# Kernel optimization log

Measured on AMD Instinct MI355X. Metric: run time of the kernel, lower is better.

The kernel has to match this reference:

```python
import jax, jax.numpy as jnp
import numpy as np

EPS = 1e-5

def _layernorm(x, gamma, beta):
    # LayerNormalization over last axis (channels), epsilon=1e-5
    mu = jnp.mean(x, axis=-1, keepdims=True)
    var = jnp.var(x, axis=-1, keepdims=True)
    return (x - mu) * jax.lax.rsqrt(var + EPS) * gamma + beta

def setup_inputs() -> dict:
    key = jax.random.key(0)
    ks = jax.random.split(key, 6)
    B, H, W, C = 8, 64, 64, 256
    std = 0.1  # NIN init_scale
    return {
        "x": jax.random.normal(ks[0], (B, H, W, C), dtype=jnp.float32),
        "ln_gamma": jnp.ones((C,), dtype=jnp.float32),
        "ln_beta": jnp.zeros((C,), dtype=jnp.float32),
        "wq": jax.random.normal(ks[1], (C, C), dtype=jnp.float32) * std,
        "bq": jnp.zeros((C,), dtype=jnp.float32),
        "wk": jax.random.normal(ks[2], (C, C), dtype=jnp.float32) * std,
        "bk": jnp.zeros((C,), dtype=jnp.float32),
        "wv": jax.random.normal(ks[3], (C, C), dtype=jnp.float32) * std,
        "bv": jnp.zeros((C,), dtype=jnp.float32),
        "wo": jax.random.normal(ks[4], (C, C), dtype=jnp.float32) * std,
        "bo": jnp.zeros((C,), dtype=jnp.float32),
    }

def reference(x, ln_gamma, ln_beta, wq, bq, wk, bk, wv, bv, wo, bo):
    B, H, W, C = x.shape
    h = _layernorm(x, ln_gamma, ln_beta)
    # 1x1 convs == per-pixel channel matmuls
    q = jnp.einsum('bhwc,cd->bhwd', h, wq) + bq
    k = jnp.einsum('bhwc,cd->bhwd', h, wk) + bk
    v = jnp.einsum('bhwc,cd->bhwd', h, wv) + bv
    scale = jnp.float32(C) ** -0.5
    # dense spatial attention over all H*W tokens
    w = jnp.einsum('bhwc,bijc->bhwij', q, k) * scale  # [B,H,W,H,W]
    w = jax.nn.softmax(w.reshape(B, H, W, H * W), axis=-1).reshape(B, H, W, H, W)
    h = jnp.einsum('bhwij,bijc->bhwc', w, v)
    h = jnp.einsum('bhwc,cd->bhwd', h, wo) + bo
    return x + h
```

## Files before the change

### kernel.cpp

```cpp
#include <hip/hip_runtime.h>
#include <stdint.h>

#define NB    8
#define NTOK  4096
#define TOK   32768
#define CDIM  256
#define BQ    128
#define BK    64
#define NT    (NTOK / BK)

#define KPITCH 264
#define VPITCH 68
#define KTILE_SH (BK * KPITCH)
#define VTILE_SH (CDIM * VPITCH)
#define KCH   33
#define VCH   34
#define TOTCH (KCH + VCH)

typedef __attribute__((ext_vector_type(8))) short bf16x8;
typedef __attribute__((ext_vector_type(4))) float f32x4;

#define SSCALE 0.09016844f

static __device__ __forceinline__ unsigned short f2bf(float f) {
    union { float f; unsigned u; } v; v.f = f;
    unsigned r = v.u + 0x7fffu + ((v.u >> 16) & 1u);
    return (unsigned short)(r >> 16);
}

static __device__ __forceinline__ void dma16(const unsigned short* g, unsigned short* l) {
    __builtin_amdgcn_global_load_lds(
        (const __attribute__((address_space(1))) unsigned int*)g,
        (__attribute__((address_space(3))) unsigned int*)l,
        16, 0, 0);
}

__global__ __launch_bounds__(256) void prep_kernel(
        const float* __restrict__ x,
        const float* __restrict__ gamma,
        const float* __restrict__ beta,
        const float* __restrict__ w0, const float* __restrict__ w1,
        const float* __restrict__ w2, const float* __restrict__ w3,
        unsigned short* __restrict__ h_bf,
        unsigned short* __restrict__ wt) {
    int bx = blockIdx.x;
    if (bx >= TOK / 4) {
        int id = bx - TOK / 4;
        int m = id >> 8, dd = id & 255;
        const float* src = (m == 0) ? w0 : (m == 1) ? w1 : (m == 2) ? w2 : w3;
        wt[m * (CDIM * CDIM) + dd * CDIM + threadIdx.x] = f2bf(src[threadIdx.x * CDIM + dd]);
        return;
    }
    int w = threadIdx.x >> 6;
    int lane = threadIdx.x & 63;
    int token = bx * 4 + w;
    const float4 xv = ((const float4*)(x + (size_t)token * CDIM))[lane];
    float s = xv.x + xv.y + xv.z + xv.w;
    #pragma unroll
    for (int off = 1; off < 64; off <<= 1) s += __shfl_xor(s, off, 64);
    float mean = s * (1.0f / 256.0f);
    float d0 = xv.x - mean, d1 = xv.y - mean, d2 = xv.z - mean, d3 = xv.w - mean;
    float ss = d0 * d0 + d1 * d1 + d2 * d2 + d3 * d3;
    #pragma unroll
    for (int off = 1; off < 64; off <<= 1) ss += __shfl_xor(ss, off, 64);
    float rstd = rsqrtf(ss * (1.0f / 256.0f) + 1e-5f);
    float4 g = ((const float4*)gamma)[lane];
    float4 b = ((const float4*)beta)[lane];
    ushort4 o;
    o.x = f2bf(d0 * rstd * g.x + b.x);
    o.y = f2bf(d1 * rstd * g.y + b.y);
    o.z = f2bf(d2 * rstd * g.z + b.z);
    o.w = f2bf(d3 * rstd * g.w + b.w);
    ((ushort4*)(h_bf + (size_t)token * CDIM))[lane] = o;
}

__global__ __launch_bounds__(128) void qkv_kernel(
        const unsigned short* __restrict__ h_bf,
        const unsigned short* __restrict__ wts,
        const float* __restrict__ bq,
        const float* __restrict__ bk,
        const float* __restrict__ bv,
        unsigned short* __restrict__ q_bf,
        unsigned short* __restrict__ k2,
        unsigned short* __restrict__ vt2) {
    __shared__ unsigned short VT[64][VPITCH];
    int tid = threadIdx.x;
    int w = tid >> 6, lane = tid & 63, quad = lane >> 4, l16 = lane & 15;
    int blk = blockIdx.x;
    int gy = blockIdx.y;
    int nt0 = gy * 4;
    int tok_base = blk * 64 + w * 32;

    bf16x8 afr[2][8];
    #pragma unroll
    for (int s = 0; s < 2; ++s)
        #pragma unroll
        for (int kk = 0; kk < 8; ++kk)
            afr[s][kk] = *(const bf16x8*)(h_bf + (size_t)(tok_base + s * 16 + l16) * CDIM + kk * 32 + quad * 8);

    {
        const unsigned short* wq_t = wts;
        #pragma unroll
        for (int ntl = 0; ntl < 4; ++ntl) {
            int nt = nt0 + ntl;
            f32x4 acc0 = {0.f, 0.f, 0.f, 0.f};
            f32x4 acc1 = {0.f, 0.f, 0.f, 0.f};
            #pragma unroll
            for (int kk = 0; kk < 8; ++kk) {
                bf16x8 bfr = *(const bf16x8*)(wq_t + (size_t)(nt * 16 + l16) * CDIM + kk * 32 + quad * 8);
                acc0 = __builtin_amdgcn_mfma_f32_16x16x32_bf16(afr[0][kk], bfr, acc0, 0, 0, 0);
                acc1 = __builtin_amdgcn_mfma_f32_16x16x32_bf16(afr[1][kk], bfr, acc1, 0, 0, 0);
            }
            int d = nt * 16 + l16;
            float bb = bq[d];
            #pragma unroll
            for (int r = 0; r < 4; ++r) {
                q_bf[(size_t)(tok_base + quad * 4 + r) * CDIM + d]      = f2bf((acc0[r] + bb) * SSCALE);
                q_bf[(size_t)(tok_base + 16 + quad * 4 + r) * CDIM + d] = f2bf((acc1[r] + bb) * SSCALE);
            }
        }
    }
    {
        const unsigned short* wk_t = wts + CDIM * CDIM;
        unsigned short* kdst = k2 + (size_t)blk * KTILE_SH;
        int row0 = w * 32 + quad * 4;
        #pragma unroll
        for (int ntl = 0; ntl < 4; ++ntl) {
            int nt = nt0 + ntl;
            f32x4 acc0 = {0.f, 0.f, 0.f, 0.f};
            f32x4 acc1 = {0.f, 0.f, 0.f, 0.f};
            #pragma unroll
            for (int kk = 0; kk < 8; ++kk) {
                bf16x8 bfr = *(const bf16x8*)(wk_t + (size_t)(nt * 16 + l16) * CDIM + kk * 32 + quad * 8);
                acc0 = __builtin_amdgcn_mfma_f32_16x16x32_bf16(afr[0][kk], bfr, acc0, 0, 0, 0);
                acc1 = __builtin_amdgcn_mfma_f32_16x16x32_bf16(afr[1][kk], bfr, acc1, 0, 0, 0);
            }
            int d = nt * 16 + l16;
            float bb = bk[d];
            #pragma unroll
            for (int r = 0; r < 4; ++r) {
                kdst[(size_t)(row0 + r) * KPITCH + d]      = f2bf(acc0[r] + bb);
                kdst[(size_t)(row0 + 16 + r) * KPITCH + d] = f2bf(acc1[r] + bb);
            }
        }
    }
    {
        const unsigned short* wv_t = wts + 2 * CDIM * CDIM;
        #pragma unroll
        for (int ntl = 0; ntl < 4; ++ntl) {
            int nt = nt0 + ntl;
            f32x4 acc0 = {0.f, 0.f, 0.f, 0.f};
            f32x4 acc1 = {0.f, 0.f, 0.f, 0.f};
            #pragma unroll
            for (int kk = 0; kk < 8; ++kk) {
                bf16x8 bfr = *(const bf16x8*)(wv_t + (size_t)(nt * 16 + l16) * CDIM + kk * 32 + quad * 8);
                acc0 = __builtin_amdgcn_mfma_f32_16x16x32_bf16(afr[0][kk], bfr, acc0, 0, 0, 0);
                acc1 = __builtin_amdgcn_mfma_f32_16x16x32_bf16(afr[1][kk], bfr, acc1, 0, 0, 0);
            }
            int d = nt * 16 + l16;
            float bb = bv[d];
            int dl = ntl * 16 + l16;
            #pragma unroll
            for (int r = 0; r < 4; ++r) {
                VT[dl][w * 32 + quad * 8 + r]     = f2bf(acc0[r] + bb);
                VT[dl][w * 32 + quad * 8 + 4 + r] = f2bf(acc1[r] + bb);
            }
        }
    }
    __syncthreads();
    const uint4* src = (const uint4*)(&VT[0][0]);
    uint4* dst = (uint4*)(vt2 + (size_t)blk * VTILE_SH + (size_t)gy * 64 * VPITCH);
    #pragma unroll
    for (int i = 0; i < 4; ++i)
        dst[i * 128 + tid] = src[i * 128 + tid];
    if (tid < 32) dst[512 + tid] = src[512 + tid];
}

#define DMA_TILE(KS, VS, ktn)                                                        \
    {                                                                                \
        const unsigned short* gk = k2 + (size_t)(b * NT + (ktn)) * KTILE_SH;         \
        const unsigned short* gv = vt2 + (size_t)(b * NT + (ktn)) * VTILE_SH;        \
        for (int c = w; c < TOTCH; c += 8) {                                         \
            if (c < KCH) dma16(gk + c * 512 + lane * 8, &KS[0][0] + c * 512);        \
            else dma16(gv + (c - KCH) * 512 + lane * 8, &VS[0][0] + (c - KCH) * 512);\
        }                                                                            \
    }

#define COMPUTE_TILE(KS, VS)                                                         \
    {                                                                                \
        f32x4 sfr[2][2];                                                             \
        _Pragma("unroll")                                                            \
        for (int nt = 0; nt < 2; ++nt) {                                             \
            f32x4 a0 = {0.f, 0.f, 0.f, 0.f};                                         \
            f32x4 a1 = {0.f, 0.f, 0.f, 0.f};                                         \
            _Pragma("unroll")                                                        \
            for (int kk = 0; kk < 8; ++kk) {                                         \
                bf16x8 kb = *(const bf16x8*)(&KS[kh * 32 + nt * 16 + l16][kk * 32 + quad * 8]); \
                a0 = __builtin_amdgcn_mfma_f32_16x16x32_bf16(kb, qfr[0][kk], a0, 0, 0, 0);      \
                a1 = __builtin_amdgcn_mfma_f32_16x16x32_bf16(kb, qfr[1][kk], a1, 0, 0, 0);      \
            }                                                                        \
            sfr[0][nt] = a0; sfr[1][nt] = a1;                                        \
        }                                                                            \
        int4 pwv[2];                                                                 \
        _Pragma("unroll")                                                            \
        for (int s = 0; s < 2; ++s) {                                                \
            unsigned pw[4];                                                          \
            _Pragma("unroll")                                                        \
            for (int nt = 0; nt < 2; ++nt)                                           \
                _Pragma("unroll")                                                    \
                for (int h = 0; h < 2; ++h) {                                        \
                    float plo = exp2f(sfr[s][nt][2 * h]);                            \
                    float phi = exp2f(sfr[s][nt][2 * h + 1]);                        \
                    lacc[s] += plo + phi;                                            \
                    pw[nt * 2 + h] = (__float_as_uint(plo) >> 16)                    \
                                   | (__float_as_uint(phi) & 0xffff0000u);           \
                }                                                                    \
            pwv[s] = make_int4(pw[0], pw[1], pw[2], pw[3]);                          \
        }                                                                            \
        bf16x8 pfr0 = *(bf16x8*)&pwv[0];                                             \
        bf16x8 pfr1 = *(bf16x8*)&pwv[1];                                             \
        _Pragma("unroll")                                                            \
        for (int nt2 = 0; nt2 < 16; ++nt2) {                                         \
            bf16x8 vb = *(const bf16x8*)(&VS[nt2 * 16 + l16][kh * 32 + quad * 8]);   \
            O[0][nt2] = __builtin_amdgcn_mfma_f32_16x16x32_bf16(pfr0, vb, O[0][nt2], 0, 0, 0);  \
            O[1][nt2] = __builtin_amdgcn_mfma_f32_16x16x32_bf16(pfr1, vb, O[1][nt2], 0, 0, 0);  \
        }                                                                            \
    }

__global__ __launch_bounds__(512, 2) void flash_kernel(
        const unsigned short* __restrict__ q_bf,
        const unsigned short* __restrict__ k2,
        const unsigned short* __restrict__ vt2,
        unsigned short* __restrict__ attn) {
    __shared__ unsigned short Ks0[BK][KPITCH];
    __shared__ unsigned short Ks1[BK][KPITCH];
    __shared__ unsigned short Vs0[CDIM][VPITCH];
    __shared__ unsigned short Vs1[CDIM][VPITCH];
    __shared__ float sLbuf[512];

    int tid = threadIdx.x;
    int w = tid >> 6, lane = tid & 63, quad = lane >> 4, l16 = lane & 15;
    int kh = w >> 2;
    int wq = w & 3;
    int bid = blockIdx.x;
    int b = bid & 7;
    int qtile = bid >> 3;
    int qrow = qtile * BQ + wq * 32;
    const size_t bbase = (size_t)b * NTOK * CDIM;

    bf16x8 qfr[2][8];
    #pragma unroll
    for (int s = 0; s < 2; ++s)
        #pragma unroll
        for (int kk = 0; kk < 8; ++kk)
            qfr[s][kk] = *(const bf16x8*)(q_bf + bbase + (size_t)(qrow + s * 16 + l16) * CDIM + kk * 32 + quad * 8);

    f32x4 O[2][16];
    #pragma unroll
    for (int s = 0; s < 2; ++s)
        #pragma unroll
        for (int i = 0; i < 16; ++i) O[s][i] = (f32x4){0.f, 0.f, 0.f, 0.f};
    float lacc[2] = {0.f, 0.f};

    DMA_TILE(Ks0, Vs0, 0);
    __syncthreads();

    for (int kt2 = 0; kt2 < NT; kt2 += 2) {
        DMA_TILE(Ks1, Vs1, kt2 + 1);
        COMPUTE_TILE(Ks0, Vs0);
        __syncthreads();
        if (kt2 + 2 < NT) DMA_TILE(Ks0, Vs0, kt2 + 2);
        COMPUTE_TILE(Ks1, Vs1);
        __syncthreads();
    }

    float* sO = (wq == 0) ? (float*)&Ks0[0][0] : (wq == 1) ? (float*)&Ks1[0][0]
              : (wq == 2) ? (float*)&Vs0[0][0] : (float*)&Vs1[0][0];
    float* sL = sLbuf + wq * 128;

    if (kh == 1) {
        #pragma unroll
        for (int s = 0; s < 2; ++s) {
            #pragma unroll
            for (int nt2 = 0; nt2 < 16; ++nt2)
                #pragma unroll
                for (int r = 0; r < 4; ++r)
                    sO[((s * 16 + nt2) * 4 + r) * 64 + lane] = O[s][nt2][r];
            sL[s * 64 + lane] = lacc[s];
        }
    }
    __syncthreads();
    if (kh == 0) {
        float lr[2][4];
        #pragma unroll
        for (int s = 0; s < 2; ++s) {
            float ls = lacc[s] + sL[s * 64 + lane];
            ls += __shfl_xor(ls, 16, 64);
            ls += __shfl_xor(ls, 32, 64);
            float li = 1.0f / ls;
            #pragma unroll
            for (int r = 0; r < 4; ++r)
                lr[s][r] = __shfl(li, quad * 4 + r, 64);
        }
        #pragma unroll
        for (int s = 0; s < 2; ++s)
            #pragma unroll
            for (int nt2 = 0; nt2 < 16; ++nt2) {
                int d = nt2 * 16 + l16;
                #pragma unroll
                for (int r = 0; r < 4; ++r) {
                    float val = (O[s][nt2][r] + sO[((s * 16 + nt2) * 4 + r) * 64 + lane]) * lr[s][r];
                    attn[bbase + (size_t)(qrow + s * 16 + quad * 4 + r) * CDIM + d] = f2bf(val);
                }
            }
    }
}

__global__ __launch_bounds__(128) void oproj_kernel(
        const unsigned short* __restrict__ attn,
        const unsigned short* __restrict__ wo_t,
        const float* __restrict__ bo,
        const float* __restrict__ x,
        float* __restrict__ out) {
    int w = threadIdx.x >> 6, lane = threadIdx.x & 63;
    int quad = lane >> 4, l16 = lane & 15;
    int tok_base = blockIdx.x * 64 + w * 32;
    int nt0 = blockIdx.y * 8;

    bf16x8 afr[2][8];
    #pragma unroll
    for (int s = 0; s < 2; ++s)
        #pragma unroll
        for (int kk = 0; kk < 8; ++kk)
            afr[s][kk] = *(const bf16x8*)(attn + (size_t)(tok_base + s * 16 + l16) * CDIM + kk * 32 + quad * 8);

    #pragma unroll
    for (int ntl = 0; ntl < 8; ++ntl) {
        int nt = nt0 + ntl;
        f32x4 acc0 = {0.f, 0.f, 0.f, 0.f};
        f32x4 acc1 = {0.f, 0.f, 0.f, 0.f};
        #pragma unroll
        for (int kk = 0; kk < 8; ++kk) {
            bf16x8 bfr = *(const bf16x8*)(wo_t + (size_t)(nt * 16 + l16) * CDIM + kk * 32 + quad * 8);
            acc0 = __builtin_amdgcn_mfma_f32_16x16x32_bf16(afr[0][kk], bfr, acc0, 0, 0, 0);
            acc1 = __builtin_amdgcn_mfma_f32_16x16x32_bf16(afr[1][kk], bfr, acc1, 0, 0, 0);
        }
        int d = nt * 16 + l16;
        float bb = bo[d];
        #pragma unroll
        for (int r = 0; r < 4; ++r) {
            size_t idx0 = (size_t)(tok_base + quad * 4 + r) * CDIM + d;
            size_t idx1 = (size_t)(tok_base + 16 + quad * 4 + r) * CDIM + d;
            out[idx0] = x[idx0] + acc0[r] + bb;
            out[idx1] = x[idx1] + acc1[r] + bb;
        }
    }
}

extern "C" void kernel_launch(void* const* d_in, const int* in_sizes, int n_in,
                              void* d_out, int out_size, void* d_ws, size_t ws_size,
                              hipStream_t stream) {
    const float* x     = (const float*)d_in[0];
    const float* gamma = (const float*)d_in[1];
    const float* beta  = (const float*)d_in[2];
    const float* wq    = (const float*)d_in[3];
    const float* bq    = (const float*)d_in[4];
    const float* wk    = (const float*)d_in[5];
    const float* bk    = (const float*)d_in[6];
    const float* wv    = (const float*)d_in[7];
    const float* bv    = (const float*)d_in[8];
    const float* wo    = (const float*)d_in[9];
    const float* bo    = (const float*)d_in[10];
    float* out = (float*)d_out;

    char* ws = (char*)d_ws;
    unsigned short* h_bf = (unsigned short*)(ws);
    unsigned short* q_bf = (unsigned short*)(ws + 16777216);
    unsigned short* k2   = (unsigned short*)(ws + 33554432);
    unsigned short* vt2  = (unsigned short*)(ws + 50855936);
    unsigned short* wt   = (unsigned short*)(ws + 68681728);
    unsigned short* attn = h_bf;

    prep_kernel<<<TOK / 4 + 1024, 256, 0, stream>>>(x, gamma, beta, wq, wk, wv, wo, h_bf, wt);
    qkv_kernel<<<dim3(TOK / 64, 4), 128, 0, stream>>>(h_bf, wt, bq, bk, bv, q_bf, k2, vt2);
    flash_kernel<<<(NTOK / BQ) * NB, 512, 0, stream>>>(q_bf, k2, vt2, attn);
    oproj_kernel<<<dim3(TOK / 64, 2), 128, 0, stream>>>(attn, wt + 3 * (CDIM * CDIM), bo, x, out);
}
```

Before: 363.4 us.

## Overlap attention tile DMA with partial waitcnt barriers, vectorize projection epilogues

The attention loop's __syncthreads calls become inline-asm barriers. A barrier before compute waits only until the previous tile's async loads have landed (vmcnt(8)), and the barrier after compute waits only for LDS reads (lgkmcnt). This keeps the next tile's DMA in flight while the current tile is computed. Separately, the QKV and output projections swap the MFMA operands so each lane holds four consecutive output channels, which allows 8- and 16-byte vectorized stores and vectorized loads of bias and residual. The hand-written vmcnt threshold depends on how many loads each wave issues per tile and on compiler ordering, so the synchronisation could be fragile.

```diff
diff --git a/kernel.cpp b/kernel.cpp
--- a/kernel.cpp
+++ b/kernel.cpp
@@ -108,22 +108,24 @@
             #pragma unroll
             for (int kk = 0; kk < 8; ++kk) {
                 bf16x8 bfr = *(const bf16x8*)(wq_t + (size_t)(nt * 16 + l16) * CDIM + kk * 32 + quad * 8);
-                acc0 = __builtin_amdgcn_mfma_f32_16x16x32_bf16(afr[0][kk], bfr, acc0, 0, 0, 0);
-                acc1 = __builtin_amdgcn_mfma_f32_16x16x32_bf16(afr[1][kk], bfr, acc1, 0, 0, 0);
+                acc0 = __builtin_amdgcn_mfma_f32_16x16x32_bf16(bfr, afr[0][kk], acc0, 0, 0, 0);
+                acc1 = __builtin_amdgcn_mfma_f32_16x16x32_bf16(bfr, afr[1][kk], acc1, 0, 0, 0);
             }
-            int d = nt * 16 + l16;
-            float bb = bq[d];
-            #pragma unroll
-            for (int r = 0; r < 4; ++r) {
-                q_bf[(size_t)(tok_base + quad * 4 + r) * CDIM + d]      = f2bf((acc0[r] + bb) * SSCALE);
-                q_bf[(size_t)(tok_base + 16 + quad * 4 + r) * CDIM + d] = f2bf((acc1[r] + bb) * SSCALE);
-            }
+            int d0 = nt * 16 + quad * 4;
+            float4 b4 = *(const float4*)(bq + d0);
+            ushort4 o0, o1;
+            o0.x = f2bf((acc0[0] + b4.x) * SSCALE); o0.y = f2bf((acc0[1] + b4.y) * SSCALE);
+            o0.z = f2bf((acc0[2] + b4.z) * SSCALE); o0.w = f2bf((acc0[3] + b4.w) * SSCALE);
+            o1.x = f2bf((acc1[0] + b4.x) * SSCALE); o1.y = f2bf((acc1[1] + b4.y) * SSCALE);
+            o1.z = f2bf((acc1[2] + b4.z) * SSCALE); o1.w = f2bf((acc1[3] + b4.w) * SSCALE);
+            *(ushort4*)(q_bf + (size_t)(tok_base + l16) * CDIM + d0)      = o0;
+            *(ushort4*)(q_bf + (size_t)(tok_base + 16 + l16) * CDIM + d0) = o1;
         }
     }
     {
         const unsigned short* wk_t = wts + CDIM * CDIM;
         unsigned short* kdst = k2 + (size_t)blk * KTILE_SH;
-        int row0 = w * 32 + quad * 4;
+        int key0 = w * 32 + l16;
         #pragma unroll
         for (int ntl = 0; ntl < 4; ++ntl) {
             int nt = nt0 + ntl;
@@ -132,16 +134,18 @@
             #pragma unroll
             for (int kk = 0; kk < 8; ++kk) {
                 bf16x8 bfr = *(const bf16x8*)(wk_t + (size_t)(nt * 16 + l16) * CDIM + kk * 32 + quad * 8);
-                acc0 = __builtin_amdgcn_mfma_f32_16x16x32_bf16(afr[0][kk], bfr, acc0, 0, 0, 0);
-                acc1 = __builtin_amdgcn_mfma_f32_16x16x32_bf16(afr[1][kk], bfr, acc1, 0, 0, 0);
+                acc0 = __builtin_amdgcn_mfma_f32_16x16x32_bf16(bfr, afr[0][kk], acc0, 0, 0, 0);
+                acc1 = __builtin_amdgcn_mfma_f32_16x16x32_bf16(bfr, afr[1][kk], acc1, 0, 0, 0);
             }
-            int d = nt * 16 + l16;
-            float bb = bk[d];
-            #pragma unroll
-            for (int r = 0; r < 4; ++r) {
-                kdst[(size_t)(row0 + r) * KPITCH + d]      = f2bf(acc0[r] + bb);
-                kdst[(size_t)(row0 + 16 + r) * KPITCH + d] = f2bf(acc1[r] + bb);
-            }
+            int d0 = nt * 16 + quad * 4;
+            float4 b4 = *(const float4*)(bk + d0);
+            ushort4 o0, o1;
+            o0.x = f2bf(acc0[0] + b4.x); o0.y = f2bf(acc0[1] + b4.y);
+            o0.z = f2bf(acc0[2] + b4.z); o0.w = f2bf(acc0[3] + b4.w);
+            o1.x = f2bf(acc1[0] + b4.x); o1.y = f2bf(acc1[1] + b4.y);
+            o1.z = f2bf(acc1[2] + b4.z); o1.w = f2bf(acc1[3] + b4.w);
+            *(ushort4*)(kdst + (size_t)key0 * KPITCH + d0)        = o0;
+            *(ushort4*)(kdst + (size_t)(key0 + 16) * KPITCH + d0) = o1;
         }
     }
     {
@@ -185,6 +189,10 @@
             else dma16(gv + (c - KCH) * 512 + lane * 8, &VS[0][0] + (c - KCH) * 512);\
         }                                                                            \
     }
+
+#define WAIT_TILE() asm volatile("s_waitcnt vmcnt(8)\n\ts_barrier" ::: "memory");
+#define WAIT_ALL()  asm volatile("s_waitcnt vmcnt(0)\n\ts_barrier" ::: "memory");
+#define READ_DONE() asm volatile("s_waitcnt lgkmcnt(0)\n\ts_barrier" ::: "memory");
 
 #define COMPUTE_TILE(KS, VS)                                                         \
     {                                                                                \
@@ -263,15 +271,20 @@
     float lacc[2] = {0.f, 0.f};
 
     DMA_TILE(Ks0, Vs0, 0);
-    __syncthreads();
 
     for (int kt2 = 0; kt2 < NT; kt2 += 2) {
         DMA_TILE(Ks1, Vs1, kt2 + 1);
+        WAIT_TILE()
         COMPUTE_TILE(Ks0, Vs0);
-        __syncthreads();
-        if (kt2 + 2 < NT) DMA_TILE(Ks0, Vs0, kt2 + 2);
+        READ_DONE()
+        if (kt2 + 2 < NT) {
+            DMA_TILE(Ks0, Vs0, kt2 + 2);
+            WAIT_TILE()
+        } else {
+            WAIT_ALL()
+        }
         COMPUTE_TILE(Ks1, Vs1);
-        __syncthreads();
+        READ_DONE()
     }
 
     float* sO = (wq == 0) ? (float*)&Ks0[0][0] : (wq == 1) ? (float*)&Ks1[0][0]
@@ -342,18 +355,22 @@
         #pragma unroll
         for (int kk = 0; kk < 8; ++kk) {
             bf16x8 bfr = *(const bf16x8*)(wo_t + (size_t)(nt * 16 + l16) * CDIM + kk * 32 + quad * 8);
-            acc0 = __builtin_amdgcn_mfma_f32_16x16x32_bf16(afr[0][kk], bfr, acc0, 0, 0, 0);
-            acc1 = __builtin_amdgcn_mfma_f32_16x16x32_bf16(afr[1][kk], bfr, acc1, 0, 0, 0);
-        }
-        int d = nt * 16 + l16;
-        float bb = bo[d];
-        #pragma unroll
-        for (int r = 0; r < 4; ++r) {
-            size_t idx0 = (size_t)(tok_base + quad * 4 + r) * CDIM + d;
-            size_t idx1 = (size_t)(tok_base + 16 + quad * 4 + r) * CDIM + d;
-            out[idx0] = x[idx0] + acc0[r] + bb;
-            out[idx1] = x[idx1] + acc1[r] + bb;
-        }
+            acc0 = __builtin_amdgcn_mfma_f32_16x16x32_bf16(bfr, afr[0][kk], acc0, 0, 0, 0);
+            acc1 = __builtin_amdgcn_mfma_f32_16x16x32_bf16(bfr, afr[1][kk], acc1, 0, 0, 0);
+        }
+        int d0 = nt * 16 + quad * 4;
+        float4 b4 = *(const float4*)(bo + d0);
+        size_t i0 = (size_t)(tok_base + l16) * CDIM + d0;
+        size_t i1 = (size_t)(tok_base + 16 + l16) * CDIM + d0;
+        float4 x0 = *(const float4*)(x + i0);
+        float4 x1 = *(const float4*)(x + i1);
+        float4 o0, o1;
+        o0.x = x0.x + acc0[0] + b4.x; o0.y = x0.y + acc0[1] + b4.y;
+        o0.z = x0.z + acc0[2] + b4.z; o0.w = x0.w + acc0[3] + b4.w;
+        o1.x = x1.x + acc1[0] + b4.x; o1.y = x1.y + acc1[1] + b4.y;
+        o1.z = x1.z + acc1[2] + b4.z; o1.w = x1.w + acc1[3] + b4.w;
+        *(float4*)(out + i0) = o0;
+        *(float4*)(out + i1) = o1;
     }
 }
 
```

Measured after the change: 366.4 us. About the same (+0.8%).
